# Optimization experiments

Hardware: AMD Instinct MI355X
Metric: run time of the kernel (lower is better)

## Reference

```python
import jax, jax.numpy as jnp
import numpy as np

B, T, H, L, D_IN = 512, 4096, 10, 8, 1


def setup_inputs() -> dict:
    key = jax.random.key(0)
    ks = jax.random.split(key, 8)
    s = 1.0 / np.sqrt(H)  # torch nn.RNN init bound
    u = lambda k, shape: jax.random.uniform(k, shape, jnp.float32, -s, s)
    return {
        "x": jax.random.normal(ks[0], (B, T, D_IN), jnp.float32),
        "h0": jnp.zeros((L, B, H), jnp.float32),
        "w_ih0": u(ks[1], (H, D_IN)),          # weight_ih_l0
        "w_ih_rest": u(ks[2], (L - 1, H, H)),  # weight_ih_l1..l7
        "w_hh": u(ks[3], (L, H, H)),           # weight_hh_l0..l7
        "b_ih": u(ks[4], (L, H)),
        "b_hh": u(ks[5], (L, H)),
        "w_lin": u(ks[6], (1, H)),
        "b_lin": u(ks[7], (1,)),
    }


def _run_layer(inp, W_ih, W_hh, bi, bh, h_init):
    # inp: [B,T,D] -> output [B,T,H], final state [B,H]
    # input projection is time-parallel; only the h@W_hh recurrence is scanned
    proj = jnp.einsum('btd,hd->bth', inp, W_ih) + bi + bh  # [B,T,H]

    def step(h, p_t):
        h_new = jnp.tanh(p_t + h @ W_hh.T)
        return h_new, h_new

    hT, ys = jax.lax.scan(step, h_init, jnp.swapaxes(proj, 0, 1))  # ys: [T,B,H]
    return jnp.swapaxes(ys, 0, 1), hT


def reference(x, h0, w_ih0, w_ih_rest, w_hh, b_ih, b_hh, w_lin, b_lin):
    out = x
    finals = []
    for l in range(L):  # fixed small layer count
        W_ih = w_ih0 if l == 0 else w_ih_rest[l - 1]
        out, hT = _run_layer(out, W_ih, w_hh[l], b_ih[l], b_hh[l], h0[l])
        finals.append(hT)
    h1 = jnp.stack(finals)            # [L,B,H]
    y = out @ w_lin.T + b_lin         # [B,T,1]
    return y, h1
```

## Files before the change

### kernel.cpp

```cpp
#include <hip/hip_runtime.h>

#define TT 4096
#define NB 512
#define NH 10
#define NL 8
#define KS 16
#define NTI (TT/KS)
#define NI (NTI + NL - 1)

typedef float v2f __attribute__((ext_vector_type(2)));

__device__ __forceinline__ v2f pk_fma(v2f a, v2f b, v2f c) {
    v2f d;
    asm("v_pk_fma_f32 %0, %1, %2, %3" : "=v"(d) : "v"(a), "v"(b), "v"(c));
    return d;
}

__device__ __forceinline__ float dpp_xor1(float v) {
    return __int_as_float(__builtin_amdgcn_update_dpp(
        __float_as_int(v), __float_as_int(v), 0xB1, 0xF, 0xF, false));
}
__device__ __forceinline__ float dpp_xor2(float v) {
    return __int_as_float(__builtin_amdgcn_update_dpp(
        __float_as_int(v), __float_as_int(v), 0x4E, 0xF, 0xF, false));
}
__device__ __forceinline__ float dpp_xor4(float v) {
    int t = __builtin_amdgcn_update_dpp(
        __float_as_int(v), __float_as_int(v), 0x104, 0xF, 0x5, false);
    t = __builtin_amdgcn_update_dpp(
        t, __float_as_int(v), 0x114, 0xF, 0xA, false);
    return __int_as_float(t);
}
__device__ __forceinline__ float dpp_xor8_hi(float v) {
    return __int_as_float(__builtin_amdgcn_update_dpp(
        __float_as_int(v), __float_as_int(v), 0x128, 0xC, 0xF, false));
}
__device__ __forceinline__ float half_sum(float z) {
    float a = z, bq = z;
    asm volatile("s_nop 1\n\tv_permlane32_swap_b32 %0, %1"
                 : "+v"(a), "+v"(bq));
    return a + bq;
}

__global__ __launch_bounds__(512, 1)
void rnn_pipe(const float* __restrict__ x, const float* __restrict__ h0,
              const float* __restrict__ w_ih0, const float* __restrict__ w_ih_rest,
              const float* __restrict__ w_hh, const float* __restrict__ b_ih,
              const float* __restrict__ b_hh, const float* __restrict__ w_lin,
              const float* __restrict__ b_lin, float* __restrict__ out)
{
    __shared__ float pbuf[2][NL-1][64][18];

    const int tid  = threadIdx.x;
    const int wv   = tid >> 6;
    const int lane = tid & 63;
    const int half = lane >> 5;
    const int bg   = (lane >> 4) & 1;
    const int h    = lane & 15;
    const int b    = blockIdx.x * 2 + bg;
    const int off  = half << 3;

    const float SC = 2.8853900817779268f;

    v2f WZ[4];
    v2f WN[4];
    float w0s = 0.f, bias2h = 0.f, bias2p = 0.f;
    const float blin = b_lin[0];

    #pragma unroll
    for (int j = 0; j < 8; ++j) {
        const int src = h ^ j ^ off;
        float wz = (h < NH && src < NH) ? SC * w_hh[(wv*NH + h)*NH + src] : 0.f;
        float wn;
        if (wv < NL-1)
            wn = (h < NH && src < NH) ? SC * w_ih_rest[(wv*NH + h)*NH + src] : 0.f;
        else
            wn = (src < NH) ? w_lin[src] : 0.f;
        if (j & 1) { WZ[j >> 1].y = wz; WN[j >> 1].y = wn; }
        else       { WZ[j >> 1].x = wz; WN[j >> 1].x = wn; }
    }
    if (h < NH && half == 0) {
        const float bb = SC * (b_ih[wv*NH + h] + b_hh[wv*NH + h]);
        if (wv == 0) { w0s = SC * w_ih0[h]; bias2p = bb; }
        else bias2h = bb;
    }
    const v2f BIAS2 = {0.f, bias2h};
    const v2f ZERO2 = {0.f, 0.f};
    const v2f W0S2  = {w0s, w0s};
    const v2f BIASP2= {bias2p, bias2p};

    const size_t hbase = ((size_t)wv*NB + b)*NH;
    v2f R[4];
    #pragma unroll
    for (int j = 0; j < 8; ++j) {
        const int src = h ^ j ^ off;
        const float v = (src < NH) ? h0[hbase + src] : 0.f;
        if (j & 1) R[j >> 1].y = v; else R[j >> 1].x = v;
    }

    const int bpbase = (lane & 48) << 2;
    float xc = 0.f, xn = 0.f, yst = 0.f, th = 0.f;
    if (wv == 0) xn = x[(size_t)b*TT + h];

    for (int i = 0; i < NI; ++i) {
        if ((unsigned)(i - wv) < (unsigned)NTI) {
            const int t0 = (i - wv) * KS;
            const int wr = i & 1, rd = wr ^ 1;

            v2f pp[8];
            if (wv == 0) {
                xc = xn;
                const int tn = t0 + KS;
                xn = (tn < TT) ? x[(size_t)b*TT + tn + h] : 0.f;
                #pragma unroll
                for (int j = 0; j < 8; ++j) {
                    const float xs0 = __uint_as_float(__builtin_amdgcn_ds_bpermute(
                        bpbase + ((2*j) << 2), __float_as_uint(xc)));
                    const float xs1 = __uint_as_float(__builtin_amdgcn_ds_bpermute(
                        bpbase + ((2*j+1) << 2), __float_as_uint(xc)));
                    pp[j] = pk_fma(W0S2, (v2f){xs0, xs1}, BIASP2);
                }
            } else {
                const v2f* prow = (const v2f*)&pbuf[rd][wv-1][lane][0];
                #pragma unroll
                for (int j = 0; j < 8; ++j) pp[j] = prow[j];
            }
            v2f nps[8];

            #pragma unroll
            for (int k = 0; k < KS; ++k) {
                v2f az = pk_fma(WZ[0], R[0], BIAS2);
                az = pk_fma(WZ[1], R[1], az);
                az = pk_fma(WZ[2], R[2], az);
                az = pk_fma(WZ[3], R[3], az);
                const float pk_ = (k & 1) ? pp[k >> 1].y : pp[k >> 1].x;
                const float zp = (az.x + pk_) + az.y;
                const float z  = half_sum(zp);
                const float u  = __builtin_amdgcn_exp2f(z);
                th = fmaf(-2.f, __builtin_amdgcn_rcpf(u + 1.f), 1.f);

                const float t0r = dpp_xor8_hi(th);
                R[0].x = t0r;
                R[0].y = dpp_xor1(t0r);
                R[1].x = dpp_xor2(t0r);
                R[1].y = dpp_xor2(R[0].y);
                const float t4r = dpp_xor4(t0r);
                R[2].x = t4r;
                R[2].y = dpp_xor1(t4r);
                R[3].x = dpp_xor2(t4r);
                R[3].y = dpp_xor2(R[2].y);

                v2f an = pk_fma(WN[0], R[0], ZERO2);
                an = pk_fma(WN[1], R[1], an);
                an = pk_fma(WN[2], R[2], an);
                an = pk_fma(WN[3], R[3], an);
                const float np = an.x + an.y;
                if (k & 1) nps[k >> 1].y = np;
                else       nps[k >> 1].x = np;
            }

            if (wv < NL-1) {
                v2f* pwr = (v2f*)&pbuf[wr][wv][lane][0];
                #pragma unroll
                for (int j = 0; j < 8; ++j) pwr[j] = nps[j];
            } else {
                #pragma unroll
                for (int k = 0; k < KS; ++k) {
                    const float np = (k & 1) ? nps[k >> 1].y : nps[k >> 1].x;
                    const float y = half_sum(np) + blin;
                    if (h == k) yst = y;
                }
                if (lane < 32)
                    out[(size_t)b*TT + t0 + h] = yst;
            }
            if (t0 + KS == TT && lane < 32 && h < NH)
                out[(size_t)NB*TT + ((size_t)wv*NB + b)*NH + h] = th;
        }
        __syncthreads();
    }
}

extern "C" void kernel_launch(void* const* d_in, const int* in_sizes, int n_in,
                              void* d_out, int out_size, void* d_ws, size_t ws_size,
                              hipStream_t stream) {
    const float* x         = (const float*)d_in[0];
    const float* h0        = (const float*)d_in[1];
    const float* w_ih0     = (const float*)d_in[2];
    const float* w_ih_rest = (const float*)d_in[3];
    const float* w_hh      = (const float*)d_in[4];
    const float* b_ih      = (const float*)d_in[5];
    const float* b_hh      = (const float*)d_in[6];
    const float* w_lin     = (const float*)d_in[7];
    const float* b_lin     = (const float*)d_in[8];
    float* out = (float*)d_out;

    rnn_pipe<<<dim3(NB / 2), dim3(512), 0, stream>>>(
        x, h0, w_ih0, w_ih_rest, w_hh, b_ih, b_hh, w_lin, b_lin, out);
}
```

Before: 682.6 us.

## Fuse recurrent and next-layer projections into shared packed FMA chain, double chunk size

Packs the recurrent weight and the next-layer input weight into one v2f per column and uses op_sel packed FMAs, so a single 8-instruction chain per step computes both the current-step recurrence and the previous step's next-layer projection. This removes the separate 4-FMA projection chain and its horizontal add from each step. The time chunk doubles from 16 to 32, which halves the number of block-wide barriers, and the pipeline buffer moves to dynamic LDS with padding. The cost is more registers for the 32-entry pp/nps arrays, a longer pipeline fill across the 8 layer waves, and more LDS.

```diff
diff --git a/kernel.cpp b/kernel.cpp
--- a/kernel.cpp
+++ b/kernel.cpp
@@ -4,12 +4,26 @@
 #define NB 512
 #define NH 10
 #define NL 8
-#define KS 16
+#define KS 32
+#define PADK 34
 #define NTI (TT/KS)
 #define NI (NTI + NL - 1)
+#define LDSBYTES (2*(NL-1)*64*PADK*4)
 
 typedef float v2f __attribute__((ext_vector_type(2)));
 
+__device__ __forceinline__ v2f pk_fma_blo(v2f a, v2f b, v2f c) {
+    v2f d;
+    asm("v_pk_fma_f32 %0, %1, %2, %3 op_sel:[0,0,0] op_sel_hi:[1,0,1]"
+        : "=v"(d) : "v"(a), "v"(b), "v"(c));
+    return d;
+}
+__device__ __forceinline__ v2f pk_fma_bhi(v2f a, v2f b, v2f c) {
+    v2f d;
+    asm("v_pk_fma_f32 %0, %1, %2, %3 op_sel:[0,1,0] op_sel_hi:[1,1,1]"
+        : "=v"(d) : "v"(a), "v"(b), "v"(c));
+    return d;
+}
 __device__ __forceinline__ v2f pk_fma(v2f a, v2f b, v2f c) {
     v2f d;
     asm("v_pk_fma_f32 %0, %1, %2, %3" : "=v"(d) : "v"(a), "v"(b), "v"(c));
@@ -49,7 +63,7 @@
               const float* __restrict__ b_hh, const float* __restrict__ w_lin,
               const float* __restrict__ b_lin, float* __restrict__ out)
 {
-    __shared__ float pbuf[2][NL-1][64][18];
+    extern __shared__ float pbuf[];
 
     const int tid  = threadIdx.x;
     const int wv   = tid >> 6;
@@ -59,33 +73,31 @@
     const int h    = lane & 15;
     const int b    = blockIdx.x * 2 + bg;
     const int off  = half << 3;
+    const int slot = (half << 4) | h;
 
     const float SC = 2.8853900817779268f;
 
-    v2f WZ[4];
-    v2f WN[4];
+    v2f WP[8];
     float w0s = 0.f, bias2h = 0.f, bias2p = 0.f;
     const float blin = b_lin[0];
 
     #pragma unroll
-    for (int j = 0; j < 8; ++j) {
-        const int src = h ^ j ^ off;
+    for (int m = 0; m < 8; ++m) {
+        const int src = h ^ m ^ off;
         float wz = (h < NH && src < NH) ? SC * w_hh[(wv*NH + h)*NH + src] : 0.f;
         float wn;
         if (wv < NL-1)
             wn = (h < NH && src < NH) ? SC * w_ih_rest[(wv*NH + h)*NH + src] : 0.f;
         else
             wn = (src < NH) ? w_lin[src] : 0.f;
-        if (j & 1) { WZ[j >> 1].y = wz; WN[j >> 1].y = wn; }
-        else       { WZ[j >> 1].x = wz; WN[j >> 1].x = wn; }
+        WP[m] = (v2f){wz, wn};
     }
     if (h < NH && half == 0) {
         const float bb = SC * (b_ih[wv*NH + h] + b_hh[wv*NH + h]);
         if (wv == 0) { w0s = SC * w_ih0[h]; bias2p = bb; }
         else bias2h = bb;
     }
-    const v2f BIAS2 = {0.f, bias2h};
-    const v2f ZERO2 = {0.f, 0.f};
+    const v2f DSEED = {bias2h, 0.f};
     const v2f W0S2  = {w0s, w0s};
     const v2f BIASP2= {bias2p, bias2p};
 
@@ -98,45 +110,62 @@
         if (j & 1) R[j >> 1].y = v; else R[j >> 1].x = v;
     }
 
-    const int bpbase = (lane & 48) << 2;
+    float* prow_rd = pbuf + (((size_t)0)              );
+    const int rdbase = (wv > 0) ? (wv-1)*64 + lane : lane;
+    const int wrbase = (wv < NL-1 ? wv : 0)*64 + lane;
+    const int PARITY = (NL-1)*64*PADK;
+
     float xc = 0.f, xn = 0.f, yst = 0.f, th = 0.f;
-    if (wv == 0) xn = x[(size_t)b*TT + h];
+    if (wv == 0) xn = x[(size_t)b*TT + slot];
 
     for (int i = 0; i < NI; ++i) {
         if ((unsigned)(i - wv) < (unsigned)NTI) {
             const int t0 = (i - wv) * KS;
             const int wr = i & 1, rd = wr ^ 1;
 
-            v2f pp[8];
+            v2f pp[KS/2];
             if (wv == 0) {
                 xc = xn;
                 const int tn = t0 + KS;
-                xn = (tn < TT) ? x[(size_t)b*TT + tn + h] : 0.f;
-                #pragma unroll
-                for (int j = 0; j < 8; ++j) {
-                    const float xs0 = __uint_as_float(__builtin_amdgcn_ds_bpermute(
-                        bpbase + ((2*j) << 2), __float_as_uint(xc)));
-                    const float xs1 = __uint_as_float(__builtin_amdgcn_ds_bpermute(
-                        bpbase + ((2*j+1) << 2), __float_as_uint(xc)));
+                xn = (tn < TT) ? x[(size_t)b*TT + tn + slot] : 0.f;
+                const int bgs = bg << 4;
+                #pragma unroll
+                for (int j = 0; j < KS/2; ++j) {
+                    const int k0 = 2*j, k1 = 2*j + 1;
+                    const int a0 = ((((k0 >> 4) << 5) | bgs | (k0 & 15)) << 2);
+                    const int a1 = ((((k1 >> 4) << 5) | bgs | (k1 & 15)) << 2);
+                    const float xs0 = __uint_as_float(
+                        __builtin_amdgcn_ds_bpermute(a0, __float_as_uint(xc)));
+                    const float xs1 = __uint_as_float(
+                        __builtin_amdgcn_ds_bpermute(a1, __float_as_uint(xc)));
                     pp[j] = pk_fma(W0S2, (v2f){xs0, xs1}, BIASP2);
                 }
             } else {
-                const v2f* prow = (const v2f*)&pbuf[rd][wv-1][lane][0];
-                #pragma unroll
-                for (int j = 0; j < 8; ++j) pp[j] = prow[j];
-            }
-            v2f nps[8];
+                const v2f* prow = (const v2f*)(pbuf + rd*PARITY + rdbase*PADK);
+                #pragma unroll
+                for (int j = 0; j < KS/2; ++j) pp[j] = prow[j];
+            }
+            v2f nps[KS/2];
 
             #pragma unroll
             for (int k = 0; k < KS; ++k) {
-                v2f az = pk_fma(WZ[0], R[0], BIAS2);
-                az = pk_fma(WZ[1], R[1], az);
-                az = pk_fma(WZ[2], R[2], az);
-                az = pk_fma(WZ[3], R[3], az);
+                v2f acc = pk_fma_blo(WP[0], R[0], DSEED);
+                acc = pk_fma_bhi(WP[1], R[0], acc);
+                acc = pk_fma_blo(WP[2], R[1], acc);
+                acc = pk_fma_bhi(WP[3], R[1], acc);
+                acc = pk_fma_blo(WP[4], R[2], acc);
+                acc = pk_fma_bhi(WP[5], R[2], acc);
+                acc = pk_fma_blo(WP[6], R[3], acc);
+                acc = pk_fma_bhi(WP[7], R[3], acc);
+
+                if (k > 0) {
+                    if ((k-1) & 1) nps[(k-1) >> 1].y = acc.y;
+                    else           nps[(k-1) >> 1].x = acc.y;
+                }
                 const float pk_ = (k & 1) ? pp[k >> 1].y : pp[k >> 1].x;
-                const float zp = (az.x + pk_) + az.y;
-                const float z  = half_sum(zp);
-                const float u  = __builtin_amdgcn_exp2f(z);
+                const float zp  = acc.x + pk_;
+                const float z   = half_sum(zp);
+                const float u   = __builtin_amdgcn_exp2f(z);
                 th = fmaf(-2.f, __builtin_amdgcn_rcpf(u + 1.f), 1.f);
 
                 const float t0r = dpp_xor8_hi(th);
@@ -149,29 +178,31 @@
                 R[2].y = dpp_xor1(t4r);
                 R[3].x = dpp_xor2(t4r);
                 R[3].y = dpp_xor2(R[2].y);
-
-                v2f an = pk_fma(WN[0], R[0], ZERO2);
-                an = pk_fma(WN[1], R[1], an);
-                an = pk_fma(WN[2], R[2], an);
-                an = pk_fma(WN[3], R[3], an);
-                const float np = an.x + an.y;
-                if (k & 1) nps[k >> 1].y = np;
-                else       nps[k >> 1].x = np;
+            }
+            {
+                v2f acc = pk_fma_blo(WP[0], R[0], DSEED);
+                acc = pk_fma_bhi(WP[1], R[0], acc);
+                acc = pk_fma_blo(WP[2], R[1], acc);
+                acc = pk_fma_bhi(WP[3], R[1], acc);
+                acc = pk_fma_blo(WP[4], R[2], acc);
+                acc = pk_fma_bhi(WP[5], R[2], acc);
+                acc = pk_fma_blo(WP[6], R[3], acc);
+                acc = pk_fma_bhi(WP[7], R[3], acc);
+                nps[(KS-1) >> 1].y = acc.y;
             }
 
             if (wv < NL-1) {
-                v2f* pwr = (v2f*)&pbuf[wr][wv][lane][0];
-                #pragma unroll
-                for (int j = 0; j < 8; ++j) pwr[j] = nps[j];
+                v2f* pwr = (v2f*)(pbuf + wr*PARITY + wrbase*PADK);
+                #pragma unroll
+                for (int j = 0; j < KS/2; ++j) pwr[j] = nps[j];
             } else {
                 #pragma unroll
-                for (int k = 0; k < KS; ++k) {
-                    const float np = (k & 1) ? nps[k >> 1].y : nps[k >> 1].x;
-                    const float y = half_sum(np) + blin;
-                    if (h == k) yst = y;
+                for (int j = 0; j < KS; ++j) {
+                    const float nv = (j & 1) ? nps[j >> 1].y : nps[j >> 1].x;
+                    const float y  = half_sum(nv) + blin;
+                    if (slot == j) yst = y;
                 }
-                if (lane < 32)
-                    out[(size_t)b*TT + t0 + h] = yst;
+                out[(size_t)b*TT + t0 + slot] = yst;
             }
             if (t0 + KS == TT && lane < 32 && h < NH)
                 out[(size_t)NB*TT + ((size_t)wv*NB + b)*NH + h] = th;
@@ -194,6 +225,9 @@
     const float* b_lin     = (const float*)d_in[8];
     float* out = (float*)d_out;
 
-    rnn_pipe<<<dim3(NB / 2), dim3(512), 0, stream>>>(
+    hipFuncSetAttribute(reinterpret_cast<const void*>(&rnn_pipe),
+                        hipFuncAttributeMaxDynamicSharedMemorySize, LDSBYTES);
+
+    rnn_pipe<<<dim3(NB / 2), dim3(512), LDSBYTES, stream>>>(
         x, h0, w_ih0, w_ih_rest, w_hh, b_ih, b_hh, w_lin, b_lin, out);
 }
```

Measured after the change: 650.5 us. 1.05x faster.
